# Optimization experiments

Measured on AMD Instinct MI355X. Metric: run time of the kernel, lower is better.

The kernel has to match this reference:

```python
import jax, jax.numpy as jnp
import numpy as np

D = 128   # embedding_dim
H = 256   # hidden_dim

def setup_inputs() -> dict:
    key = jax.random.key(0)
    ks = jax.random.split(key, 16)
    s = 0.02
    B, N = 4, 384
    inp = {
        "cities": jax.random.uniform(ks[0], (B, N, 2), dtype=jnp.float32),
        # city_encoder: Linear(2,H) -> ReLU -> Linear(H,D); weights stored [in,out]
        "We1": jax.random.normal(ks[1], (2, H), dtype=jnp.float32) * s,
        "be1": jnp.zeros((H,), jnp.float32),
        "We2": jax.random.normal(ks[2], (H, D), dtype=jnp.float32) * s,
        "be2": jnp.zeros((D,), jnp.float32),
        # attention: Linear(D,H) -> ReLU -> Linear(H,1)
        "Wa1": jax.random.normal(ks[3], (D, H), dtype=jnp.float32) * s,
        "ba1": jnp.zeros((H,), jnp.float32),
        "wa2": jax.random.normal(ks[4], (H, 1), dtype=jnp.float32) * s,
        "ba2": jnp.zeros((1,), jnp.float32),
        # decoder: Linear(2D,H) -> ReLU -> Linear(H,1) -> Sigmoid
        "Wd1": jax.random.normal(ks[5], (2 * D, H), dtype=jnp.float32) * s,
        "bd1": jnp.zeros((H,), jnp.float32),
        "wd2": jax.random.normal(ks[6], (H, 1), dtype=jnp.float32) * s,
        "bd2": jnp.zeros((1,), jnp.float32),
    }
    return inp


def reference(cities, We1, be1, We2, be2, Wa1, ba1, wa2, ba2, Wd1, bd1, wd2, bd2):
    B, N, _ = cities.shape
    # city encoder MLP: [B,N,2] -> [B,N,D]
    emb = jax.nn.relu(cities @ We1 + be1) @ We2 + be2
    # attention scores -> softmax over cities
    att = jax.nn.softmax((jax.nn.relu(emb @ Wa1 + ba1) @ wa2 + ba2).squeeze(-1), axis=1)
    # Pairwise decoder: concat(e_i, e_j) @ Wd1 == e_i @ Wd1[:D] + e_j @ Wd1[D:]
    Ai = emb @ Wd1[:D]   # [B,N,H] contribution of row city i
    Aj = emb @ Wd1[D:]   # [B,N,H] contribution of col city j
    h = jax.nn.relu(Ai[:, :, None, :] + Aj[:, None, :, :] + bd1)  # [B,N,N,H]
    p = jax.nn.sigmoid((h @ wd2).squeeze(-1) + bd2)               # [B,N,N]
    # diagonal (i == j) was never written in the torch loop -> stays 0
    p = p * (1.0 - jnp.eye(N, dtype=p.dtype))
    return att, p
```

## Files before the change

kernel.cpp:

```cpp
#include <hip/hip_runtime.h>
#include <hip/hip_fp16.h>
#include <math.h>

#define NCITY 384
#define BATCH 4
#define DIM   128
#define HID   256
#define M_TOT (BATCH * NCITY)
#define TR    6

#define CHUNK_FLOATS 32768

__device__ __forceinline__ unsigned pk_add(unsigned a, unsigned b) {
    unsigned r;
    asm("v_pk_add_f16 %0, %1, %2" : "=v"(r) : "v"(a), "v"(b));
    return r;
}
__device__ __forceinline__ unsigned pk_max0(unsigned a) {
    unsigned r;
    asm("v_pk_max_f16 %0, %1, %2" : "=v"(r) : "v"(a), "v"(0u));
    return r;
}
__device__ __forceinline__ unsigned pk_fma(unsigned a, unsigned b, unsigned c) {
    unsigned r;
    asm("v_pk_fma_f16 %0, %1, %2, %3" : "=v"(r) : "v"(a), "v"(b), "v"(c));
    return r;
}
__device__ __forceinline__ unsigned pack2(float a, float b) {
    union { __half2 h2; unsigned u; } c;
    c.h2 = __float22half2_rn(make_float2(a, b));
    return c.u;
}
__device__ __forceinline__ float sum2(unsigned u) {
    union { unsigned u; __half2 h2; } c;
    c.u = u;
    return __low2float(c.h2) + __high2float(c.h2);
}

__device__ __forceinline__ void stage128(const float* __restrict__ gsrc,
                                         float* lbuf, int tid)
{
    const int lane = tid & 63;
    const int wv   = tid >> 6;
    #pragma unroll
    for (int i = 0; i < 32; ++i) {
        const int slot = i * 4 + wv;
        __builtin_amdgcn_global_load_lds(
            (const __attribute__((address_space(1))) void*)(gsrc + slot * 256 + lane * 4),
            (__attribute__((address_space(3))) void*)(lbuf + slot * 256),
            16, 0, 0);
    }
}

__device__ __forceinline__ void chunk_gemm(float* wbuf,
                                           const float (*emb_s)[DIM],
                                           int tid, float out6[TR])
{
    const int c4 = tid & 63;
    const int wv = tid >> 6;
    const int k0 = wv * 32;

    float4 acc[TR];
    #pragma unroll
    for (int rr = 0; rr < TR; ++rr) { acc[rr].x = 0.f; acc[rr].y = 0.f; acc[rr].z = 0.f; acc[rr].w = 0.f; }

    #pragma unroll 2
    for (int kb = 0; kb < 32; kb += 4) {
        float4 ev[TR];
        #pragma unroll
        for (int rr = 0; rr < TR; ++rr)
            ev[rr] = *(const float4*)&emb_s[rr][k0 + kb];
        #pragma unroll
        for (int kk = 0; kk < 4; ++kk) {
            const float4 w4 = *(const float4*)&wbuf[(k0 + kb + kk) * HID + c4 * 4];
            #pragma unroll
            for (int rr = 0; rr < TR; ++rr) {
                const float e = ((const float*)&ev[rr])[kk];
                acc[rr].x = fmaf(e, w4.x, acc[rr].x);
                acc[rr].y = fmaf(e, w4.y, acc[rr].y);
                acc[rr].z = fmaf(e, w4.z, acc[rr].z);
                acc[rr].w = fmaf(e, w4.w, acc[rr].w);
            }
        }
    }
    __syncthreads();
    #pragma unroll
    for (int rr = 0; rr < TR; ++rr)
        *(float4*)&wbuf[(wv * TR + rr) * HID + c4 * 4] = acc[rr];
    __syncthreads();
    #pragma unroll
    for (int rr = 0; rr < TR; ++rr)
        out6[rr] = wbuf[(0 * TR + rr) * HID + tid] + wbuf[(1 * TR + rr) * HID + tid]
                 + wbuf[(2 * TR + rr) * HID + tid] + wbuf[(3 * TR + rr) * HID + tid];
}

__global__ __launch_bounds__(256) void encoder_kernel(
    const float* __restrict__ cities,
    const float* __restrict__ We1, const float* __restrict__ be1,
    const float* __restrict__ We2, const float* __restrict__ be2,
    const float* __restrict__ Wa1, const float* __restrict__ ba1,
    const float* __restrict__ wa2, const float* __restrict__ ba2,
    const float* __restrict__ Wd1, const float* __restrict__ bd1,
    float* __restrict__ score, float* __restrict__ Ai, float* __restrict__ Aj)
{
    __shared__ float wbuf[CHUNK_FLOATS];
    __shared__ float h1_s[TR][HID];
    __shared__ float emb_s[TR][DIM];
    __shared__ float red2[4][TR];

    const int tid = threadIdx.x;
    const int r0  = blockIdx.x * TR;

    stage128(We2, wbuf, tid);

    {
        const float w0 = We1[tid], w1 = We1[HID + tid], b = be1[tid];
        #pragma unroll
        for (int rr = 0; rr < TR; ++rr) {
            const float cx = cities[(r0 + rr) * 2];
            const float cy = cities[(r0 + rr) * 2 + 1];
            h1_s[rr][tid] = fmaxf(fmaf(cx, w0, fmaf(cy, w1, b)), 0.f);
        }
    }
    __syncthreads();

    {
        const int d4 = tid & 31;
        const int ks = tid >> 5;
        const int k0 = ks * 32;
        float4 acc[TR];
        #pragma unroll
        for (int rr = 0; rr < TR; ++rr) { acc[rr].x = 0.f; acc[rr].y = 0.f; acc[rr].z = 0.f; acc[rr].w = 0.f; }

        #pragma unroll 2
        for (int kb = 0; kb < 32; kb += 4) {
            float4 hv[TR];
            #pragma unroll
            for (int rr = 0; rr < TR; ++rr)
                hv[rr] = *(const float4*)&h1_s[rr][k0 + kb];
            #pragma unroll
            for (int kk = 0; kk < 4; ++kk) {
                const float4 w4 = *(const float4*)&wbuf[(k0 + kb + kk) * DIM + d4 * 4];
                #pragma unroll
                for (int rr = 0; rr < TR; ++rr) {
                    const float h = ((const float*)&hv[rr])[kk];
                    acc[rr].x = fmaf(h, w4.x, acc[rr].x);
                    acc[rr].y = fmaf(h, w4.y, acc[rr].y);
                    acc[rr].z = fmaf(h, w4.z, acc[rr].z);
                    acc[rr].w = fmaf(h, w4.w, acc[rr].w);
                }
            }
        }
        #pragma unroll
        for (int rr = 0; rr < TR; ++rr) {
            acc[rr].x += __shfl_xor(acc[rr].x, 32);
            acc[rr].y += __shfl_xor(acc[rr].y, 32);
            acc[rr].z += __shfl_xor(acc[rr].z, 32);
            acc[rr].w += __shfl_xor(acc[rr].w, 32);
        }
        __syncthreads();
        if ((tid & 63) < 32) {
            const int wv = tid >> 6;
            #pragma unroll
            for (int rr = 0; rr < TR; ++rr)
                *(float4*)&wbuf[(wv * TR + rr) * DIM + d4 * 4] = acc[rr];
        }
        __syncthreads();
        for (int o = tid; o < TR * DIM; o += 256) {
            const int rr = o >> 7, d = o & (DIM - 1);
            emb_s[rr][d] = wbuf[(0 * TR + rr) * DIM + d] + wbuf[(1 * TR + rr) * DIM + d]
                         + wbuf[(2 * TR + rr) * DIM + d] + wbuf[(3 * TR + rr) * DIM + d]
                         + be2[d];
        }
        __syncthreads();
    }

    stage128(Wa1, wbuf, tid);
    __syncthreads();
    {
        float o6[TR];
        chunk_gemm(wbuf, emb_s, tid, o6);
        const float ba1v = ba1[tid], wa2v = wa2[tid];
        const int wv = tid >> 6;
        #pragma unroll
        for (int rr = 0; rr < TR; ++rr) {
            float v = fmaxf(o6[rr] + ba1v, 0.f) * wa2v;
            #pragma unroll
            for (int off = 32; off > 0; off >>= 1)
                v += __shfl_down(v, off);
            if ((tid & 63) == 0) red2[wv][rr] = v;
        }
        __syncthreads();
        if (tid < TR)
            score[r0 + tid] = red2[0][tid] + red2[1][tid] + red2[2][tid] + red2[3][tid];
    }

    stage128(Wd1, wbuf, tid);
    __syncthreads();
    {
        float o6[TR];
        chunk_gemm(wbuf, emb_s, tid, o6);
        const float bd1v = bd1[tid];
        #pragma unroll
        for (int rr = 0; rr < TR; ++rr)
            Ai[(r0 + rr) * HID + tid] = o6[rr] + bd1v;
        __syncthreads();
    }

    stage128(Wd1 + DIM * HID, wbuf, tid);
    __syncthreads();
    {
        float o6[TR];
        chunk_gemm(wbuf, emb_s, tid, o6);
        #pragma unroll
        for (int rr = 0; rr < TR; ++rr)
            Aj[(r0 + rr) * HID + tid] = o6[rr];
    }
}

union H8 { float4 f4; unsigned u[4]; };

__global__ __launch_bounds__(256) void pair_sm_kernel(
    const float* __restrict__ Ai, const float* __restrict__ Aj,
    const float* __restrict__ wd2, const float* __restrict__ bd2,
    const float* __restrict__ score, float* __restrict__ att,
    float* __restrict__ p)
{
    const int tid = threadIdx.x;
    const int b   = blockIdx.y;

    if (blockIdx.x == 144) {
        __shared__ float red[8];
        const int t = tid;
        const float v0 = score[b * NCITY + t];
        const bool  h2v = (t < NCITY - 256);
        const float v1 = h2v ? score[b * NCITY + 256 + t] : -3.4e38f;
        float m = fmaxf(v0, v1);
        #pragma unroll
        for (int off = 32; off > 0; off >>= 1)
            m = fmaxf(m, __shfl_down(m, off));
        if ((t & 63) == 0) red[t >> 6] = m;
        __syncthreads();
        m = fmaxf(fmaxf(red[0], red[1]), fmaxf(red[2], red[3]));
        const float e0 = __expf(v0 - m);
        const float e1 = h2v ? __expf(v1 - m) : 0.f;
        float s = e0 + e1;
        #pragma unroll
        for (int off = 32; off > 0; off >>= 1)
            s += __shfl_down(s, off);
        if ((t & 63) == 0) red[4 + (t >> 6)] = s;
        __syncthreads();
        s = red[4] + red[5] + red[6] + red[7];
        att[b * NCITY + t] = e0 / s;
        if (h2v) att[b * NCITY + 256 + t] = e1 / s;
        return;
    }

    __shared__ __half ai_s[32 * HID];
    __shared__ __half aj_s[32 * HID];
    __shared__ unsigned wd2h[HID / 2];

    const int i0 = (blockIdx.x / 12) * 32;
    const int j0 = (blockIdx.x % 12) * 32;

    if (tid < HID / 2) {
        const float2 w2 = *(const float2*)&wd2[tid * 2];
        wd2h[tid] = pack2(w2.x, w2.y);
    }

    for (int u = tid; u < 32 * 32; u += 256) {
        const int r = u >> 5, s = u & 31;
        const int su = (s ^ (r & 15)) * 8;
        {
            const int g = (b * NCITY + i0 + r) * HID + s * 8;
            const float4 f0 = *(const float4*)&Ai[g];
            const float4 f1 = *(const float4*)&Ai[g + 4];
            H8 pk;
            pk.u[0] = pack2(f0.x, f0.y);
            pk.u[1] = pack2(f0.z, f0.w);
            pk.u[2] = pack2(f1.x, f1.y);
            pk.u[3] = pack2(f1.z, f1.w);
            *(float4*)&ai_s[r * HID + su] = pk.f4;
        }
        {
            const int g = (b * NCITY + j0 + r) * HID + s * 8;
            const float4 f0 = *(const float4*)&Aj[g];
            const float4 f1 = *(const float4*)&Aj[g + 4];
            H8 pk;
            pk.u[0] = pack2(f0.x, f0.y);
            pk.u[1] = pack2(f0.z, f0.w);
            pk.u[2] = pack2(f1.x, f1.y);
            pk.u[3] = pack2(f1.z, f1.w);
            *(float4*)&aj_s[r * HID + su] = pk.f4;
        }
    }
    __syncthreads();

    const int tx = tid & 15;
    const int ty = tid >> 4;

    unsigned a00A = 0u, a00B = 0u, a01A = 0u, a01B = 0u;
    unsigned a10A = 0u, a10B = 0u, a11A = 0u, a11B = 0u;

    #pragma unroll 4
    for (int k8 = 0; k8 < 32; ++k8) {
        const int ci = (k8 ^ ty) * 8;
        const int cj = (k8 ^ tx) * 8;
        H8 x0, x1, y0, y1;
        x0.f4 = *(const float4*)&ai_s[ ty       * HID + ci];
        x1.f4 = *(const float4*)&ai_s[(ty + 16) * HID + ci];
        y0.f4 = *(const float4*)&aj_s[ tx       * HID + cj];
        y1.f4 = *(const float4*)&aj_s[(tx + 16) * HID + cj];

        #pragma unroll
        for (int q = 0; q < 4; ++q) {
            const unsigned w = wd2h[k8 * 4 + q];
            const unsigned t00 = pk_max0(pk_add(x0.u[q], y0.u[q]));
            const unsigned t01 = pk_max0(pk_add(x0.u[q], y1.u[q]));
            const unsigned t10 = pk_max0(pk_add(x1.u[q], y0.u[q]));
            const unsigned t11 = pk_max0(pk_add(x1.u[q], y1.u[q]));
            if (q < 2) {
                a00A = pk_fma(t00, w, a00A);
                a01A = pk_fma(t01, w, a01A);
                a10A = pk_fma(t10, w, a10A);
                a11A = pk_fma(t11, w, a11A);
            } else {
                a00B = pk_fma(t00, w, a00B);
                a01B = pk_fma(t01, w, a01B);
                a10B = pk_fma(t10, w, a10B);
                a11B = pk_fma(t11, w, a11B);
            }
        }
    }

    const float bd = bd2[0];
    float accs[2][2];
    accs[0][0] = sum2(a00A) + sum2(a00B);
    accs[0][1] = sum2(a01A) + sum2(a01B);
    accs[1][0] = sum2(a10A) + sum2(a10B);
    accs[1][1] = sum2(a11A) + sum2(a11B);

    #pragma unroll
    for (int ii = 0; ii < 2; ++ii) {
        #pragma unroll
        for (int jj = 0; jj < 2; ++jj) {
            const int gi = i0 + ty + ii * 16;
            const int gj = j0 + tx + jj * 16;
            const float v = 1.f / (1.f + __expf(-(accs[ii][jj] + bd)));
            p[(b * NCITY + gi) * NCITY + gj] = (gi == gj) ? 0.f : v;
        }
    }
}

extern "C" void kernel_launch(void* const* d_in, const int* in_sizes, int n_in,
                              void* d_out, int out_size, void* d_ws, size_t ws_size,
                              hipStream_t stream)
{
    const float* cities = (const float*)d_in[0];
    const float* We1    = (const float*)d_in[1];
    const float* be1    = (const float*)d_in[2];
    const float* We2    = (const float*)d_in[3];
    const float* be2    = (const float*)d_in[4];
    const float* Wa1    = (const float*)d_in[5];
    const float* ba1    = (const float*)d_in[6];
    const float* wa2    = (const float*)d_in[7];
    const float* ba2    = (const float*)d_in[8];
    const float* Wd1    = (const float*)d_in[9];
    const float* bd1    = (const float*)d_in[10];
    const float* wd2    = (const float*)d_in[11];
    const float* bd2    = (const float*)d_in[12];
    (void)ba2;

    float* out_att = (float*)d_out;
    float* out_p   = out_att + BATCH * NCITY;

    float* score = (float*)d_ws;
    float* Ai    = score + M_TOT;
    float* Aj    = Ai + M_TOT * HID;

    encoder_kernel<<<M_TOT / TR, 256, 0, stream>>>(
        cities, We1, be1, We2, be2, Wa1, ba1, wa2, ba2, Wd1, bd1,
        score, Ai, Aj);

    pair_sm_kernel<<<dim3(145, BATCH), 256, 0, stream>>>(
        Ai, Aj, wd2, bd2, score, out_att, out_p);
}
```

Measured before the change: 37.58 us.

## Double-buffer encoder weight staging to overlap global-to-LDS loads with GEMM

Splits each 128KB weight stage in the encoder kernel into two 64KB halves held in separate LDS buffers. The next half is loaded into one buffer while the other is being consumed, using explicit vmcnt waits and raw barriers in place of __syncthreads. The aim is to hide global-to-LDS load latency behind the FMA loops of the encoder's GEMM stages. Parameter loads are also hoisted to the start of the kernel. In exchange, correctness now depends on hand-written waitcnt counts and barrier placement.

```diff
diff --git a/kernel.cpp b/kernel.cpp
--- a/kernel.cpp
+++ b/kernel.cpp
@@ -9,41 +9,24 @@
 #define M_TOT (BATCH * NCITY)
 #define TR    6
 
-#define CHUNK_FLOATS 32768
-
-__device__ __forceinline__ unsigned pk_add(unsigned a, unsigned b) {
-    unsigned r;
-    asm("v_pk_add_f16 %0, %1, %2" : "=v"(r) : "v"(a), "v"(b));
-    return r;
-}
-__device__ __forceinline__ unsigned pk_max0(unsigned a) {
-    unsigned r;
-    asm("v_pk_max_f16 %0, %1, %2" : "=v"(r) : "v"(a), "v"(0u));
-    return r;
-}
-__device__ __forceinline__ unsigned pk_fma(unsigned a, unsigned b, unsigned c) {
-    unsigned r;
-    asm("v_pk_fma_f16 %0, %1, %2, %3" : "=v"(r) : "v"(a), "v"(b), "v"(c));
-    return r;
-}
-__device__ __forceinline__ unsigned pack2(float a, float b) {
-    union { __half2 h2; unsigned u; } c;
-    c.h2 = __float22half2_rn(make_float2(a, b));
-    return c.u;
-}
-__device__ __forceinline__ float sum2(unsigned u) {
-    union { unsigned u; __half2 h2; } c;
-    c.u = u;
-    return __low2float(c.h2) + __high2float(c.h2);
-}
-
-__device__ __forceinline__ void stage128(const float* __restrict__ gsrc,
-                                         float* lbuf, int tid)
+#define HALF_FLOATS 16384
+
+#define VMWAIT16() do { asm volatile("s_waitcnt vmcnt(16)" ::: "memory"); \
+                        __builtin_amdgcn_sched_barrier(0); } while (0)
+#define VMWAIT0()  do { asm volatile("s_waitcnt vmcnt(0)"  ::: "memory"); \
+                        __builtin_amdgcn_sched_barrier(0); } while (0)
+#define LGKM0()    do { asm volatile("s_waitcnt lgkmcnt(0)" ::: "memory"); \
+                        __builtin_amdgcn_sched_barrier(0); } while (0)
+#define SBAR()     do { __builtin_amdgcn_s_barrier(); \
+                        __builtin_amdgcn_sched_barrier(0); } while (0)
+
+__device__ __forceinline__ void stage64(const float* __restrict__ gsrc,
+                                        float* lbuf, int tid)
 {
     const int lane = tid & 63;
     const int wv   = tid >> 6;
     #pragma unroll
-    for (int i = 0; i < 32; ++i) {
+    for (int i = 0; i < 16; ++i) {
         const int slot = i * 4 + wv;
         __builtin_amdgcn_global_load_lds(
             (const __attribute__((address_space(1))) void*)(gsrc + slot * 256 + lane * 4),
@@ -52,46 +35,74 @@
     }
 }
 
-__device__ __forceinline__ void chunk_gemm(float* wbuf,
+__device__ __forceinline__ void emb_half(const float* buf,
+                                         const float (*h1_s)[HID],
+                                         int tid, int kbase, float4 eacc[TR])
+{
+    const int d4 = tid & 31;
+    const int k0 = (tid >> 5) * 16;
+    #pragma unroll 2
+    for (int kb = 0; kb < 16; kb += 4) {
+        float4 hv[TR];
+        #pragma unroll
+        for (int rr = 0; rr < TR; ++rr)
+            hv[rr] = *(const float4*)&h1_s[rr][kbase + k0 + kb];
+        #pragma unroll
+        for (int kk = 0; kk < 4; ++kk) {
+            const float4 w4 = *(const float4*)&buf[(k0 + kb + kk) * DIM + d4 * 4];
+            #pragma unroll
+            for (int rr = 0; rr < TR; ++rr) {
+                const float h = ((const float*)&hv[rr])[kk];
+                eacc[rr].x = fmaf(h, w4.x, eacc[rr].x);
+                eacc[rr].y = fmaf(h, w4.y, eacc[rr].y);
+                eacc[rr].z = fmaf(h, w4.z, eacc[rr].z);
+                eacc[rr].w = fmaf(h, w4.w, eacc[rr].w);
+            }
+        }
+    }
+}
+
+__device__ __forceinline__ void chunk_half(const float* buf,
                                            const float (*emb_s)[DIM],
-                                           int tid, float out6[TR])
+                                           int tid, int kbase, float4 cacc[TR])
 {
     const int c4 = tid & 63;
-    const int wv = tid >> 6;
-    const int k0 = wv * 32;
-
-    float4 acc[TR];
-    #pragma unroll
-    for (int rr = 0; rr < TR; ++rr) { acc[rr].x = 0.f; acc[rr].y = 0.f; acc[rr].z = 0.f; acc[rr].w = 0.f; }
-
+    const int k0 = (tid >> 6) * 16;
     #pragma unroll 2
-    for (int kb = 0; kb < 32; kb += 4) {
+    for (int kb = 0; kb < 16; kb += 4) {
         float4 ev[TR];
         #pragma unroll
         for (int rr = 0; rr < TR; ++rr)
-            ev[rr] = *(const float4*)&emb_s[rr][k0 + kb];
+            ev[rr] = *(const float4*)&emb_s[rr][kbase + k0 + kb];
         #pragma unroll
         for (int kk = 0; kk < 4; ++kk) {
-            const float4 w4 = *(const float4*)&wbuf[(k0 + kb + kk) * HID + c4 * 4];
+            const float4 w4 = *(const float4*)&buf[(k0 + kb + kk) * HID + c4 * 4];
             #pragma unroll
             for (int rr = 0; rr < TR; ++rr) {
                 const float e = ((const float*)&ev[rr])[kk];
-                acc[rr].x = fmaf(e, w4.x, acc[rr].x);
-                acc[rr].y = fmaf(e, w4.y, acc[rr].y);
-                acc[rr].z = fmaf(e, w4.z, acc[rr].z);
-                acc[rr].w = fmaf(e, w4.w, acc[rr].w);
+                cacc[rr].x = fmaf(e, w4.x, cacc[rr].x);
+                cacc[rr].y = fmaf(e, w4.y, cacc[rr].y);
+                cacc[rr].z = fmaf(e, w4.z, cacc[rr].z);
+                cacc[rr].w = fmaf(e, w4.w, cacc[rr].w);
             }
         }
     }
-    __syncthreads();
+}
+
+__device__ __forceinline__ void chunk_reduce(float* scr, int tid,
+                                             const float4 cacc[TR], float out6[TR])
+{
+    const int c4 = tid & 63;
+    const int wv = tid >> 6;
+    SBAR();
     #pragma unroll
     for (int rr = 0; rr < TR; ++rr)
-        *(float4*)&wbuf[(wv * TR + rr) * HID + c4 * 4] = acc[rr];
-    __syncthreads();
+        *(float4*)&scr[(wv * TR + rr) * HID + c4 * 4] = cacc[rr];
+    LGKM0(); SBAR();
     #pragma unroll
     for (int rr = 0; rr < TR; ++rr)
-        out6[rr] = wbuf[(0 * TR + rr) * HID + tid] + wbuf[(1 * TR + rr) * HID + tid]
-                 + wbuf[(2 * TR + rr) * HID + tid] + wbuf[(3 * TR + rr) * HID + tid];
+        out6[rr] = scr[(0 * TR + rr) * HID + tid] + scr[(1 * TR + rr) * HID + tid]
+                 + scr[(2 * TR + rr) * HID + tid] + scr[(3 * TR + rr) * HID + tid];
 }
 
 __global__ __launch_bounds__(256) void encoder_kernel(
@@ -103,84 +114,86 @@
     const float* __restrict__ Wd1, const float* __restrict__ bd1,
     float* __restrict__ score, float* __restrict__ Ai, float* __restrict__ Aj)
 {
-    __shared__ float wbuf[CHUNK_FLOATS];
+    __shared__ float wbuf[2 * HALF_FLOATS];
     __shared__ float h1_s[TR][HID];
     __shared__ float emb_s[TR][DIM];
     __shared__ float red2[4][TR];
 
+    float* b0 = wbuf;
+    float* b1 = wbuf + HALF_FLOATS;
+
     const int tid = threadIdx.x;
     const int r0  = blockIdx.x * TR;
 
-    stage128(We2, wbuf, tid);
+    const float w0 = We1[tid], w1 = We1[HID + tid], bb1 = be1[tid];
+    const float ba1v = ba1[tid], wa2v = wa2[tid], bd1v = bd1[tid];
+    const float be2v = be2[tid & (DIM - 1)];
+    float cx[TR], cy[TR];
+    #pragma unroll
+    for (int rr = 0; rr < TR; ++rr) {
+        cx[rr] = cities[(r0 + rr) * 2];
+        cy[rr] = cities[(r0 + rr) * 2 + 1];
+    }
+    #pragma unroll
+    for (int rr = 0; rr < TR; ++rr)
+        h1_s[rr][tid] = fmaxf(fmaf(cx[rr], w0, fmaf(cy[rr], w1, bb1)), 0.f);
+    __builtin_amdgcn_sched_barrier(0);
+
+    stage64(We2,               b0, tid);
+    stage64(We2 + HALF_FLOATS, b1, tid);
+    VMWAIT16(); LGKM0(); SBAR();
+
+    float4 eacc[TR];
+    #pragma unroll
+    for (int rr = 0; rr < TR; ++rr) eacc[rr] = make_float4(0.f, 0.f, 0.f, 0.f);
+
+    emb_half(b0, h1_s, tid, 0, eacc);
+    SBAR();
+    stage64(Wa1, b0, tid);
+    VMWAIT16(); SBAR();
+    emb_half(b1, h1_s, tid, 128, eacc);
 
     {
-        const float w0 = We1[tid], w1 = We1[HID + tid], b = be1[tid];
         #pragma unroll
         for (int rr = 0; rr < TR; ++rr) {
-            const float cx = cities[(r0 + rr) * 2];
-            const float cy = cities[(r0 + rr) * 2 + 1];
-            h1_s[rr][tid] = fmaxf(fmaf(cx, w0, fmaf(cy, w1, b)), 0.f);
-        }
-    }
-    __syncthreads();
-
-    {
-        const int d4 = tid & 31;
-        const int ks = tid >> 5;
-        const int k0 = ks * 32;
-        float4 acc[TR];
-        #pragma unroll
-        for (int rr = 0; rr < TR; ++rr) { acc[rr].x = 0.f; acc[rr].y = 0.f; acc[rr].z = 0.f; acc[rr].w = 0.f; }
-
-        #pragma unroll 2
-        for (int kb = 0; kb < 32; kb += 4) {
-            float4 hv[TR];
+            eacc[rr].x += __shfl_xor(eacc[rr].x, 32);
+            eacc[rr].y += __shfl_xor(eacc[rr].y, 32);
+            eacc[rr].z += __shfl_xor(eacc[rr].z, 32);
+            eacc[rr].w += __shfl_xor(eacc[rr].w, 32);
+        }
+        SBAR();
+        if ((tid & 63) < 32) {
+            const int wv = tid >> 6, d4 = tid & 31;
             #pragma unroll
             for (int rr = 0; rr < TR; ++rr)
-                hv[rr] = *(const float4*)&h1_s[rr][k0 + kb];
-            #pragma unroll
-            for (int kk = 0; kk < 4; ++kk) {
-                const float4 w4 = *(const float4*)&wbuf[(k0 + kb + kk) * DIM + d4 * 4];
-                #pragma unroll
-                for (int rr = 0; rr < TR; ++rr) {
-                    const float h = ((const float*)&hv[rr])[kk];
-                    acc[rr].x = fmaf(h, w4.x, acc[rr].x);
-                    acc[rr].y = fmaf(h, w4.y, acc[rr].y);
-                    acc[rr].z = fmaf(h, w4.z, acc[rr].z);
-                    acc[rr].w = fmaf(h, w4.w, acc[rr].w);
-                }
-            }
-        }
-        #pragma unroll
-        for (int rr = 0; rr < TR; ++rr) {
-            acc[rr].x += __shfl_xor(acc[rr].x, 32);
-            acc[rr].y += __shfl_xor(acc[rr].y, 32);
-            acc[rr].z += __shfl_xor(acc[rr].z, 32);
-            acc[rr].w += __shfl_xor(acc[rr].w, 32);
-        }
-        __syncthreads();
-        if ((tid & 63) < 32) {
-            const int wv = tid >> 6;
-            #pragma unroll
-            for (int rr = 0; rr < TR; ++rr)
-                *(float4*)&wbuf[(wv * TR + rr) * DIM + d4 * 4] = acc[rr];
-        }
-        __syncthreads();
-        for (int o = tid; o < TR * DIM; o += 256) {
+                *(float4*)&b1[(wv * TR + rr) * DIM + d4 * 4] = eacc[rr];
+        }
+        LGKM0(); SBAR();
+        #pragma unroll
+        for (int j = 0; j < 3; ++j) {
+            const int o = tid + j * 256;
             const int rr = o >> 7, d = o & (DIM - 1);
-            emb_s[rr][d] = wbuf[(0 * TR + rr) * DIM + d] + wbuf[(1 * TR + rr) * DIM + d]
-                         + wbuf[(2 * TR + rr) * DIM + d] + wbuf[(3 * TR + rr) * DIM + d]
-                         + be2[d];
-        }
-        __syncthreads();
-    }
-
-    stage128(Wa1, wbuf, tid);
-    __syncthreads();
+            emb_s[rr][d] = b1[(0 * TR + rr) * DIM + d] + b1[(1 * TR + rr) * DIM + d]
+                         + b1[(2 * TR + rr) * DIM + d] + b1[(3 * TR + rr) * DIM + d]
+                         + be2v;
+        }
+        LGKM0(); SBAR();
+    }
+
+    float4 cacc[TR];
+    float o6[TR];
+
+    stage64(Wa1 + HALF_FLOATS, b1, tid);
+    VMWAIT16(); SBAR();
+    #pragma unroll
+    for (int rr = 0; rr < TR; ++rr) cacc[rr] = make_float4(0.f, 0.f, 0.f, 0.f);
+    chunk_half(b0, emb_s, tid, 0, cacc);
+    SBAR();
+    stage64(Wd1, b0, tid);
+    VMWAIT16(); SBAR();
+    chunk_half(b1, emb_s, tid, 64, cacc);
+    chunk_reduce(b1, tid, cacc, o6);
     {
-        float o6[TR];
-        chunk_gemm(wbuf, emb_s, tid, o6);
-        const float ba1v = ba1[tid], wa2v = wa2[tid];
         const int wv = tid >> 6;
         #pragma unroll
         for (int rr = 0; rr < TR; ++rr) {
@@ -190,32 +203,65 @@
                 v += __shfl_down(v, off);
             if ((tid & 63) == 0) red2[wv][rr] = v;
         }
-        __syncthreads();
+        LGKM0(); SBAR();
         if (tid < TR)
             score[r0 + tid] = red2[0][tid] + red2[1][tid] + red2[2][tid] + red2[3][tid];
-    }
-
-    stage128(Wd1, wbuf, tid);
-    __syncthreads();
-    {
-        float o6[TR];
-        chunk_gemm(wbuf, emb_s, tid, o6);
-        const float bd1v = bd1[tid];
-        #pragma unroll
-        for (int rr = 0; rr < TR; ++rr)
-            Ai[(r0 + rr) * HID + tid] = o6[rr] + bd1v;
-        __syncthreads();
-    }
-
-    stage128(Wd1 + DIM * HID, wbuf, tid);
-    __syncthreads();
-    {
-        float o6[TR];
-        chunk_gemm(wbuf, emb_s, tid, o6);
-        #pragma unroll
-        for (int rr = 0; rr < TR; ++rr)
-            Aj[(r0 + rr) * HID + tid] = o6[rr];
-    }
+        SBAR();
+    }
+
+    stage64(Wd1 + HALF_FLOATS, b1, tid);
+    VMWAIT16(); SBAR();
+    #pragma unroll
+    for (int rr = 0; rr < TR; ++rr) cacc[rr] = make_float4(0.f, 0.f, 0.f, 0.f);
+    chunk_half(b0, emb_s, tid, 0, cacc);
+    SBAR();
+    stage64(Wd1 + 2 * HALF_FLOATS, b0, tid);
+    VMWAIT16(); SBAR();
+    chunk_half(b1, emb_s, tid, 64, cacc);
+    chunk_reduce(b1, tid, cacc, o6);
+    #pragma unroll
+    for (int rr = 0; rr < TR; ++rr)
+        Ai[(r0 + rr) * HID + tid] = o6[rr] + bd1v;
+    SBAR();
+
+    stage64(Wd1 + 3 * HALF_FLOATS, b1, tid);
+    VMWAIT16(); SBAR();
+    #pragma unroll
+    for (int rr = 0; rr < TR; ++rr) cacc[rr] = make_float4(0.f, 0.f, 0.f, 0.f);
+    chunk_half(b0, emb_s, tid, 0, cacc);
+    VMWAIT0(); SBAR();
+    chunk_half(b1, emb_s, tid, 64, cacc);
+    chunk_reduce(b0, tid, cacc, o6);
+    #pragma unroll
+    for (int rr = 0; rr < TR; ++rr)
+        Aj[(r0 + rr) * HID + tid] = o6[rr];
+    (void)ba2;
+}
+
+__device__ __forceinline__ unsigned pk_add(unsigned a, unsigned b) {
+    unsigned r;
+    asm("v_pk_add_f16 %0, %1, %2" : "=v"(r) : "v"(a), "v"(b));
+    return r;
+}
+__device__ __forceinline__ unsigned pk_max0(unsigned a) {
+    unsigned r;
+    asm("v_pk_max_f16 %0, %1, %2" : "=v"(r) : "v"(a), "v"(0u));
+    return r;
+}
+__device__ __forceinline__ unsigned pk_fma(unsigned a, unsigned b, unsigned c) {
+    unsigned r;
+    asm("v_pk_fma_f16 %0, %1, %2, %3" : "=v"(r) : "v"(a), "v"(b), "v"(c));
+    return r;
+}
+__device__ __forceinline__ unsigned pack2(float a, float b) {
+    union { __half2 h2; unsigned u; } c;
+    c.h2 = __float22half2_rn(make_float2(a, b));
+    return c.u;
+}
+__device__ __forceinline__ float sum2(unsigned u) {
+    union { unsigned u; __half2 h2; } c;
+    c.u = u;
+    return __low2float(c.h2) + __high2float(c.h2);
 }
 
 union H8 { float4 f4; unsigned u[4]; };
@@ -369,7 +415,6 @@
     const float* bd1    = (const float*)d_in[10];
     const float* wd2    = (const float*)d_in[11];
     const float* bd2    = (const float*)d_in[12];
-    (void)ba2;
 
     float* out_att = (float*)d_out;
     float* out_p   = out_att + BATCH * NCITY;
```

Result: slower. 38.36 us (+2.1%).

## Stream encoder weights from global memory instead of staging them in LDS

Applied to the files above, without the earlier changes.

The encoder no longer copies each 128 KB weight chunk into shared memory with global_load_lds. It reads weights directly from global memory (L2/cache) inside the GEMM loops, and only a small scratch buffer stays in LDS for the cross-wave reduction. This cuts LDS use from about 130 KB to about 30 KB per block, so more blocks can share a CU (launch bounds now ask for 3), and it removes the staging barriers. The cost is that every weight read goes through the vector memory path, which may be slower per access than LDS.

```diff
diff --git a/kernel.cpp b/kernel.cpp
--- a/kernel.cpp
+++ b/kernel.cpp
@@ -1,6 +1,5 @@
 #include <hip/hip_runtime.h>
 #include <hip/hip_fp16.h>
-#include <math.h>
 
 #define NCITY 384
 #define BATCH 4
@@ -9,52 +8,9 @@
 #define M_TOT (BATCH * NCITY)
 #define TR    6
 
-#define CHUNK_FLOATS 32768
-
-__device__ __forceinline__ unsigned pk_add(unsigned a, unsigned b) {
-    unsigned r;
-    asm("v_pk_add_f16 %0, %1, %2" : "=v"(r) : "v"(a), "v"(b));
-    return r;
-}
-__device__ __forceinline__ unsigned pk_max0(unsigned a) {
-    unsigned r;
-    asm("v_pk_max_f16 %0, %1, %2" : "=v"(r) : "v"(a), "v"(0u));
-    return r;
-}
-__device__ __forceinline__ unsigned pk_fma(unsigned a, unsigned b, unsigned c) {
-    unsigned r;
-    asm("v_pk_fma_f16 %0, %1, %2, %3" : "=v"(r) : "v"(a), "v"(b), "v"(c));
-    return r;
-}
-__device__ __forceinline__ unsigned pack2(float a, float b) {
-    union { __half2 h2; unsigned u; } c;
-    c.h2 = __float22half2_rn(make_float2(a, b));
-    return c.u;
-}
-__device__ __forceinline__ float sum2(unsigned u) {
-    union { unsigned u; __half2 h2; } c;
-    c.u = u;
-    return __low2float(c.h2) + __high2float(c.h2);
-}
-
-__device__ __forceinline__ void stage128(const float* __restrict__ gsrc,
-                                         float* lbuf, int tid)
-{
-    const int lane = tid & 63;
-    const int wv   = tid >> 6;
-    #pragma unroll
-    for (int i = 0; i < 32; ++i) {
-        const int slot = i * 4 + wv;
-        __builtin_amdgcn_global_load_lds(
-            (const __attribute__((address_space(1))) void*)(gsrc + slot * 256 + lane * 4),
-            (__attribute__((address_space(3))) void*)(lbuf + slot * 256),
-            16, 0, 0);
-    }
-}
-
-__device__ __forceinline__ void chunk_gemm(float* wbuf,
-                                           const float (*emb_s)[DIM],
-                                           int tid, float out6[TR])
+__device__ __forceinline__ void chunk_stream(
+    const float* __restrict__ W,
+    const float (*emb_s)[DIM], float* scr, int tid, float out6[TR])
 {
     const int c4 = tid & 63;
     const int wv = tid >> 6;
@@ -62,7 +18,7 @@
 
     float4 acc[TR];
     #pragma unroll
-    for (int rr = 0; rr < TR; ++rr) { acc[rr].x = 0.f; acc[rr].y = 0.f; acc[rr].z = 0.f; acc[rr].w = 0.f; }
+    for (int rr = 0; rr < TR; ++rr) acc[rr] = make_float4(0.f, 0.f, 0.f, 0.f);
 
     #pragma unroll 2
     for (int kb = 0; kb < 32; kb += 4) {
@@ -72,7 +28,7 @@
             ev[rr] = *(const float4*)&emb_s[rr][k0 + kb];
         #pragma unroll
         for (int kk = 0; kk < 4; ++kk) {
-            const float4 w4 = *(const float4*)&wbuf[(k0 + kb + kk) * HID + c4 * 4];
+            const float4 w4 = *(const float4*)&W[(k0 + kb + kk) * HID + c4 * 4];
             #pragma unroll
             for (int rr = 0; rr < TR; ++rr) {
                 const float e = ((const float*)&ev[rr])[kk];
@@ -86,15 +42,15 @@
     __syncthreads();
     #pragma unroll
     for (int rr = 0; rr < TR; ++rr)
-        *(float4*)&wbuf[(wv * TR + rr) * HID + c4 * 4] = acc[rr];
+        *(float4*)&scr[(wv * TR + rr) * HID + c4 * 4] = acc[rr];
     __syncthreads();
     #pragma unroll
     for (int rr = 0; rr < TR; ++rr)
-        out6[rr] = wbuf[(0 * TR + rr) * HID + tid] + wbuf[(1 * TR + rr) * HID + tid]
-                 + wbuf[(2 * TR + rr) * HID + tid] + wbuf[(3 * TR + rr) * HID + tid];
-}
-
-__global__ __launch_bounds__(256) void encoder_kernel(
+        out6[rr] = scr[(0 * TR + rr) * HID + tid] + scr[(1 * TR + rr) * HID + tid]
+                 + scr[(2 * TR + rr) * HID + tid] + scr[(3 * TR + rr) * HID + tid];
+}
+
+__global__ __launch_bounds__(256, 3) void encoder_stream(
     const float* __restrict__ cities,
     const float* __restrict__ We1, const float* __restrict__ be1,
     const float* __restrict__ We2, const float* __restrict__ be2,
@@ -103,34 +59,31 @@
     const float* __restrict__ Wd1, const float* __restrict__ bd1,
     float* __restrict__ score, float* __restrict__ Ai, float* __restrict__ Aj)
 {
-    __shared__ float wbuf[CHUNK_FLOATS];
     __shared__ float h1_s[TR][HID];
     __shared__ float emb_s[TR][DIM];
+    __shared__ float scr[4 * TR * HID];
     __shared__ float red2[4][TR];
 
     const int tid = threadIdx.x;
     const int r0  = blockIdx.x * TR;
 
-    stage128(We2, wbuf, tid);
-
     {
-        const float w0 = We1[tid], w1 = We1[HID + tid], b = be1[tid];
+        const float w0 = We1[tid], w1 = We1[HID + tid], b1v = be1[tid];
         #pragma unroll
         for (int rr = 0; rr < TR; ++rr) {
-            const float cx = cities[(r0 + rr) * 2];
-            const float cy = cities[(r0 + rr) * 2 + 1];
-            h1_s[rr][tid] = fmaxf(fmaf(cx, w0, fmaf(cy, w1, b)), 0.f);
+            const float cxx = cities[(r0 + rr) * 2];
+            const float cyy = cities[(r0 + rr) * 2 + 1];
+            h1_s[rr][tid] = fmaxf(fmaf(cxx, w0, fmaf(cyy, w1, b1v)), 0.f);
         }
     }
     __syncthreads();
 
     {
         const int d4 = tid & 31;
-        const int ks = tid >> 5;
-        const int k0 = ks * 32;
+        const int k0 = (tid >> 5) * 32;
         float4 acc[TR];
         #pragma unroll
-        for (int rr = 0; rr < TR; ++rr) { acc[rr].x = 0.f; acc[rr].y = 0.f; acc[rr].z = 0.f; acc[rr].w = 0.f; }
+        for (int rr = 0; rr < TR; ++rr) acc[rr] = make_float4(0.f, 0.f, 0.f, 0.f);
 
         #pragma unroll 2
         for (int kb = 0; kb < 32; kb += 4) {
@@ -140,7 +93,7 @@
                 hv[rr] = *(const float4*)&h1_s[rr][k0 + kb];
             #pragma unroll
             for (int kk = 0; kk < 4; ++kk) {
-                const float4 w4 = *(const float4*)&wbuf[(k0 + kb + kk) * DIM + d4 * 4];
+                const float4 w4 = *(const float4*)&We2[(k0 + kb + kk) * DIM + d4 * 4];
                 #pragma unroll
                 for (int rr = 0; rr < TR; ++rr) {
                     const float h = ((const float*)&hv[rr])[kk];
@@ -158,28 +111,26 @@
             acc[rr].z += __shfl_xor(acc[rr].z, 32);
             acc[rr].w += __shfl_xor(acc[rr].w, 32);
         }
-        __syncthreads();
         if ((tid & 63) < 32) {
             const int wv = tid >> 6;
             #pragma unroll
             for (int rr = 0; rr < TR; ++rr)
-                *(float4*)&wbuf[(wv * TR + rr) * DIM + d4 * 4] = acc[rr];
+                *(float4*)&scr[(wv * TR + rr) * DIM + d4 * 4] = acc[rr];
         }
         __syncthreads();
         for (int o = tid; o < TR * DIM; o += 256) {
             const int rr = o >> 7, d = o & (DIM - 1);
-            emb_s[rr][d] = wbuf[(0 * TR + rr) * DIM + d] + wbuf[(1 * TR + rr) * DIM + d]
-                         + wbuf[(2 * TR + rr) * DIM + d] + wbuf[(3 * TR + rr) * DIM + d]
+            emb_s[rr][d] = scr[(0 * TR + rr) * DIM + d] + scr[(1 * TR + rr) * DIM + d]
+                         + scr[(2 * TR + rr) * DIM + d] + scr[(3 * TR + rr) * DIM + d]
                          + be2[d];
         }
         __syncthreads();
     }
 
-    stage128(Wa1, wbuf, tid);
-    __syncthreads();
+    float o6[TR];
+
+    chunk_stream(Wa1, emb_s, scr, tid, o6);
     {
-        float o6[TR];
-        chunk_gemm(wbuf, emb_s, tid, o6);
         const float ba1v = ba1[tid], wa2v = wa2[tid];
         const int wv = tid >> 6;
         #pragma unroll
@@ -195,29 +146,39 @@
             score[r0 + tid] = red2[0][tid] + red2[1][tid] + red2[2][tid] + red2[3][tid];
     }
 
-    stage128(Wd1, wbuf, tid);
-    __syncthreads();
+    chunk_stream(Wd1, emb_s, scr, tid, o6);
     {
-        float o6[TR];
-        chunk_gemm(wbuf, emb_s, tid, o6);
         const float bd1v = bd1[tid];
         #pragma unroll
         for (int rr = 0; rr < TR; ++rr)
             Ai[(r0 + rr) * HID + tid] = o6[rr] + bd1v;
-        __syncthreads();
-    }
-
-    stage128(Wd1 + DIM * HID, wbuf, tid);
-    __syncthreads();
-    {
-        float o6[TR];
-        chunk_gemm(wbuf, emb_s, tid, o6);
-        #pragma unroll
-        for (int rr = 0; rr < TR; ++rr)
-            Aj[(r0 + rr) * HID + tid] = o6[rr];
-    }
-}
-
+    }
+
+    chunk_stream(Wd1 + DIM * HID, emb_s, scr, tid, o6);
+    #pragma unroll
+    for (int rr = 0; rr < TR; ++rr)
+        Aj[(r0 + rr) * HID + tid] = o6[rr];
+    (void)ba2;
+}
+
+__device__ __forceinline__ unsigned pk_add(unsigned a, unsigned b) {
+    unsigned r; asm("v_pk_add_f16 %0, %1, %2" : "=v"(r) : "v"(a), "v"(b)); return r;
+}
+__device__ __forceinline__ unsigned pk_max0(unsigned a) {
+    unsigned r; asm("v_pk_max_f16 %0, %1, %2" : "=v"(r) : "v"(a), "v"(0u)); return r;
+}
+__device__ __forceinline__ unsigned pk_fma(unsigned a, unsigned b, unsigned c) {
+    unsigned r; asm("v_pk_fma_f16 %0, %1, %2, %3" : "=v"(r) : "v"(a), "v"(b), "v"(c)); return r;
+}
+__device__ __forceinline__ unsigned pack2(float a, float b) {
+    union { __half2 h2; unsigned u; } c;
+    c.h2 = __float22half2_rn(make_float2(a, b));
+    return c.u;
+}
+__device__ __forceinline__ float sum2(unsigned u) {
+    union { unsigned u; __half2 h2; } c; c.u = u;
+    return __low2float(c.h2) + __high2float(c.h2);
+}
 union H8 { float4 f4; unsigned u[4]; };
 
 __global__ __launch_bounds__(256) void pair_sm_kernel(
@@ -369,16 +330,15 @@
     const float* bd1    = (const float*)d_in[10];
     const float* wd2    = (const float*)d_in[11];
     const float* bd2    = (const float*)d_in[12];
-    (void)ba2;
 
     float* out_att = (float*)d_out;
-    float* out_p   = out_att + BATCH * NCITY;
+    float* out_p   = out_att + M_TOT;
 
     float* score = (float*)d_ws;
     float* Ai    = score + M_TOT;
     float* Aj    = Ai + M_TOT * HID;
 
-    encoder_kernel<<<M_TOT / TR, 256, 0, stream>>>(
+    encoder_stream<<<M_TOT / TR, 256, 0, stream>>>(
         cities, We1, be1, We2, be2, Wa1, ba1, wa2, ba2, Wd1, bd1,
         score, Ai, Aj);
 
```

New measurement: 34.01 us. 1.1x faster.
